# Kernel optimization log

Measured on AMD Instinct MI355X. Metric: run time of the kernel, lower is better.

The kernel has to match this reference:

```python
import jax, jax.numpy as jnp
import numpy as np

# --- fake-quant helpers with straight-through estimator (STE) ---

def _ste(x, xq):
    # identity grad through the rounding
    return x + jax.lax.stop_gradient(xq - x)

def act_quant(x, bit=2):
    # symmetric per-tensor uniform fake-quant of activations
    n = float(2 ** (bit - 1) - 1)  # 2-bit -> 1 level each side
    s = jnp.max(jnp.abs(x)) + 1e-8
    xq = jnp.round(jnp.clip(x / s, -1.0, 1.0) * n) / n * s
    return _ste(x, xq)

def weight_quant(w, bit=2):
    # DoReFa-style low-bit weight fake-quant
    levels = float(2 ** bit - 1)
    wt = jnp.tanh(w)
    wt = wt / (jnp.max(jnp.abs(wt)) + 1e-8)        # in [-1, 1]
    wq = 2.0 * (jnp.round((wt + 1.0) * 0.5 * levels) / levels) - 1.0
    return _ste(wt, wq)

def conv3x3(x, w, b):
    # NCHW, OIHW, stride 1, padding 1
    y = jax.lax.conv_general_dilated(
        x, w, window_strides=(1, 1), padding=((1, 1), (1, 1)),
        dimension_numbers=("NCHW", "OIHW", "NCHW"))
    return y + b[None, :, None, None]


def setup_inputs() -> dict:
    key = jax.random.key(0)
    k1, k2, k3, k4, k5 = jax.random.split(key, 5)
    B, C, H, W = 16, 64, 128, 128
    fan_in = C * 3 * 3
    std = 1.0 / np.sqrt(fan_in)
    return {
        "x": jax.random.normal(k1, (B, C, H, W), dtype=jnp.float32),
        "w1": jax.random.normal(k2, (C, C, 3, 3), dtype=jnp.float32) * std,
        "b1": jax.random.normal(k3, (C,), dtype=jnp.float32) * std,
        "w2": jax.random.normal(k4, (C, C, 3, 3), dtype=jnp.float32) * std,
        "b2": jax.random.normal(k5, (C,), dtype=jnp.float32) * std,
    }


def reference(x, w1, b1, w2, b2):
    A_BIT, W_BIT, RES_SCALE = 2, 2, 1.0
    out = act_quant(x, A_BIT)                 # quant1
    out = conv3x3(out, weight_quant(w1, W_BIT), b1)  # conv1 (low-bit)
    out1 = jax.nn.relu(out)                   # act
    out1 = act_quant(out1, A_BIT)             # quant2
    res = conv3x3(out1, weight_quant(w2, W_BIT), b2) # conv2 (low-bit)
    return res * RES_SCALE + x                # scaled residual add
```

## Files before the change

kernel.cpp:

```cpp
#include <hip/hip_runtime.h>
#include <math.h>

#define NB 16
#define CC 64
#define HH 128
#define WW 128
#define NPIX (NB*CC*HH*WW)
#define WELEM (CC*CC*9)

#define TR 16
#define TC 16
#define HR 18
#define HC 18
#define HPX (HR*HC)
#define PL  (HH*WW)

#define PYY 132
#define PXX 130
#define XQIMG (PYY*PXX*64)
#define XQTOT (NB*XQIMG)

#define S2OFF 512

typedef __attribute__((ext_vector_type(4))) int   int32x4;
typedef __attribute__((ext_vector_type(4))) short short4_t;
typedef __attribute__((ext_vector_type(8))) short short8_t;

__device__ __forceinline__ int lds_a(int pix, int q) {
    return pix * 64 + ((q ^ ((pix >> 1) & 3)) << 4);
}

__device__ __forceinline__ float read_s1(const unsigned* scal) {
    float m = 0.f;
    #pragma unroll
    for (int i = 0; i < 32; ++i) m = fmaxf(m, __uint_as_float(scal[i * 16]));
    return m + 1e-8f;
}

__device__ __forceinline__ float max4(float4 v) {
    return fmaxf(fmaxf(fabsf(v.x), fabsf(v.y)), fmaxf(fabsf(v.z), fabsf(v.w)));
}

__global__ __launch_bounds__(256) void k_reduce(const float* __restrict__ x,
                                                const float* __restrict__ w1,
                                                const float* __restrict__ w2,
                                                unsigned* __restrict__ scal,
                                                signed char* __restrict__ o1,
                                                signed char* __restrict__ o2) {
    __shared__ float red[4];
    const int tid = threadIdx.x;
    if (blockIdx.x < 2048) {
        const float4* x4 = (const float4*)x;
        const int base = blockIdx.x * 2048 + tid;
        float4 v0 = x4[base];
        float4 v1 = x4[base + 256];
        float4 v2 = x4[base + 512];
        float4 v3 = x4[base + 768];
        float4 v4 = x4[base + 1024];
        float4 v5 = x4[base + 1280];
        float4 v6 = x4[base + 1536];
        float4 v7 = x4[base + 1792];
        float a0 = fmaxf(max4(v0), max4(v1));
        float a1 = fmaxf(max4(v2), max4(v3));
        float a2 = fmaxf(max4(v4), max4(v5));
        float a3 = fmaxf(max4(v6), max4(v7));
        float m = fmaxf(fmaxf(a0, a1), fmaxf(a2, a3));
        #pragma unroll
        for (int o = 32; o; o >>= 1) m = fmaxf(m, __shfl_down(m, o, 64));
        if ((tid & 63) == 0) red[tid >> 6] = m;
        __syncthreads();
        if (tid == 0) {
            float v = fmaxf(fmaxf(red[0], red[1]), fmaxf(red[2], red[3]));
            atomicMax(&scal[(blockIdx.x & 31) * 16], __float_as_uint(v));
        }
    } else {
        const int wb = blockIdx.x - 2048;
        const int ten = wb >> 4;
        const int sl  = wb & 15;
        const float* __restrict__ w = ten ? w2 : w1;
        signed char* __restrict__ w8 = ten ? o2 : o1;

        const float4* w4 = (const float4*)w;
        float m = 0.f;
        #pragma unroll
        for (int k = 0; k < 9; ++k) {
            float4 a = w4[tid + (k * 4 + 0) * 256];
            float4 b = w4[tid + (k * 4 + 1) * 256];
            float4 c = w4[tid + (k * 4 + 2) * 256];
            float4 d = w4[tid + (k * 4 + 3) * 256];
            m = fmaxf(m, fmaxf(fmaxf(max4(a), max4(b)), fmaxf(max4(c), max4(d))));
        }
        #pragma unroll
        for (int o = 32; o; o >>= 1) m = fmaxf(m, __shfl_down(m, o, 64));
        if ((tid & 63) == 0) red[tid >> 6] = m;
        __syncthreads();
        float mx = fmaxf(fmaxf(red[0], red[1]), fmaxf(red[2], red[3]));
        float inv = 1.f / (tanhf(mx) + 1e-8f);

        #pragma unroll
        for (int j = 0; j < 9; ++j) {
            int i = sl * 2304 + j * 256 + tid;
            float wt = tanhf(w[i]) * inv;
            float r  = rintf((wt + 1.f) * 1.5f);
            int oc = i / 576, rem = i % 576, ic = rem / 9, tap = rem % 9;
            int lane2 = (oc & 15) | ((ic >> 4) << 4);
            w8[(((oc >> 4) * 9 + tap) * 64 + lane2) * 16 + (ic & 15)] =
                (signed char)(int)(2.f * r - 3.f);
        }
    }
}

__global__ __launch_bounds__(256) void k_quantx(const float* __restrict__ x,
                                                const unsigned* __restrict__ scal,
                                                signed char* __restrict__ xq) {
    __shared__ signed char ldsA[64 * 68];
    __shared__ int ldsB[64 * 16];
    const int tid = threadIdx.x;
    const int n = blockIdx.z, y = blockIdx.y, s = blockIdx.x;
    const float inv_s1 = 1.f / read_s1(scal);

    {
        const int ic = tid >> 2, g = tid & 3;
        const float* __restrict__ src =
            x + (((size_t)n * CC + ic) * HH + y) * WW + s * 64 + g * 16;
        unsigned dw[4];
        #pragma unroll
        for (int q = 0; q < 4; ++q) {
            float4 v = *(const float4*)(src + q * 4);
            float e[4] = {v.x, v.y, v.z, v.w};
            unsigned d = 0;
            #pragma unroll
            for (int j = 0; j < 4; ++j) {
                int qq = (int)rintf(fminf(fmaxf(e[j] * inv_s1, -1.f), 1.f));
                d |= (unsigned)(qq & 255) << (8 * j);
            }
            dw[q] = d;
        }
        *(int4*)(ldsA + ic * 68 + g * 16) = *(const int4*)dw;
    }
    __syncthreads();
    #pragma unroll
    for (int i = 0; i < 4; ++i) {
        int idx = tid + i * 256;
        int d = idx & 15, p = idx >> 4;
        const signed char* a = ldsA + (d * 4) * 68 + p;
        unsigned b0 = (unsigned char)a[0];
        unsigned b1 = (unsigned char)a[68];
        unsigned b2 = (unsigned char)a[136];
        unsigned b3 = (unsigned char)a[204];
        ldsB[p * 16 + d] = (int)(b0 | (b1 << 8) | (b2 << 16) | (b3 << 24));
    }
    __syncthreads();
    signed char* dst = xq + ((size_t)n * PYY + (y + 1)) * (PXX * 64)
                          + (size_t)(1 + s * 64) * 64;
    ((int4*)dst)[tid] = ((const int4*)ldsB)[tid];
}

__global__ __launch_bounds__(512, 5) void k_conv1(
    const signed char* __restrict__ xq,
    const signed char* __restrict__ w8,
    const float* __restrict__ bias,
    unsigned* __restrict__ scal,
    short* __restrict__ accout)
{
    __shared__ float redm[8];
    const int tid = threadIdx.x;
    const int n   = blockIdx.z;
    const int oy0 = blockIdx.y * TR;
    const int ox0 = blockIdx.x * TC;
    const float s1 = read_s1(scal);

    const int w     = tid >> 6;
    const int lane  = tid & 63;
    const int lq    = lane >> 4;
    const int lc    = lane & 15;
    const int mH    = w & 1;
    const int rbase = (w >> 1) * 4;

    const signed char* __restrict__ A0 = xq + (size_t)n * XQIMG
        + ((size_t)(oy0 + rbase) * PXX + ox0 + lc) * 64 + lq * 16;
    const signed char* __restrict__ W0 = w8 + ((size_t)mH * 18 * 64 + lane) * 16;

    int32x4 acc0[4] = {};
    int32x4 acc1[4] = {};
    #pragma unroll 3
    for (int tap = 0; tap < 9; ++tap) {
        const int ky = tap / 3, kx = tap % 3;
        int32x4 b0 = *(const int32x4*)(W0 + (size_t)tap * 1024);
        int32x4 b1 = *(const int32x4*)(W0 + (size_t)(9 + tap) * 1024);
        const signed char* ar = A0 + (ky * PXX + kx) * 64;
        #pragma unroll
        for (int j = 0; j < 4; ++j) {
            int32x4 a = *(const int32x4*)(ar + j * (PXX * 64));
            acc0[j] = __builtin_amdgcn_mfma_i32_16x16x64_i8(a, b0, acc0[j], 0, 0, 0);
            acc1[j] = __builtin_amdgcn_mfma_i32_16x16x64_i8(a, b1, acc1[j], 0, 0, 0);
        }
    }

    const float sc = s1 * (1.f / 3.f);
    const int oc0 = mH * 32 + lc;
    const int oc1 = oc0 + 16;
    const float bo0 = bias[oc0], bo1 = bias[oc1];
    const size_t abase = (((size_t)n * HH + (oy0 + rbase)) * WW + (ox0 + lq * 4)) * 64;

    float m2 = 0.f;
    #pragma unroll
    for (int j = 0; j < 4; ++j) {
        #pragma unroll
        for (int g = 0; g < 4; ++g) {
            int v0 = acc0[j][g], v1 = acc1[j][g];
            m2 = fmaxf(m2, sc * (float)v0 + bo0);
            m2 = fmaxf(m2, sc * (float)v1 + bo1);
            size_t a = abase + ((size_t)j * WW + g) * 64;
            accout[a + oc0] = (short)v0;
            accout[a + oc1] = (short)v1;
        }
    }
    #pragma unroll
    for (int o = 32; o; o >>= 1) m2 = fmaxf(m2, __shfl_down(m2, o, 64));
    if (lane == 0) redm[w] = m2;
    __syncthreads();
    if (tid == 0) {
        float v = redm[0];
        #pragma unroll
        for (int i = 1; i < 8; ++i) v = fmaxf(v, redm[i]);
        int slot = (blockIdx.x + blockIdx.y * 8 + blockIdx.z) & 7;
        atomicMax(&scal[S2OFF + slot * 32], __float_as_uint(v));
    }
}

__global__ __launch_bounds__(512, 5) void k_conv2(
    const float* __restrict__ x,
    const short* __restrict__ accin,
    const signed char* __restrict__ w8,
    const float* __restrict__ bias,
    const float* __restrict__ b1v,
    const unsigned* __restrict__ scal,
    float* __restrict__ out)
{
    __shared__ signed char sA[HPX * 64] __attribute__((aligned(16)));

    const int tid = threadIdx.x;
    const int n   = blockIdx.z;
    const int oy0 = blockIdx.y * TR;
    const int ox0 = blockIdx.x * TC;

    const float s1 = read_s1(scal);
    float mx = 0.f;
    #pragma unroll
    for (int i = 0; i < 8; ++i) mx = fmaxf(mx, __uint_as_float(scal[S2OFF + i * 32]));
    const float s2v = mx + 1e-8f;
    const float half_s2 = 0.5f * s2v;
    const float sc1 = s1 * (1.f / 3.f);

    for (int t = tid; t < HPX; t += 512) {
        const int r = t / HC, c = t - r * HC;
        const int y  = oy0 - 1 + r;
        const int xx = ox0 - 1 + c;
        unsigned pk[16];
        #pragma unroll
        for (int d = 0; d < 16; ++d) pk[d] = 0;
        if (y >= 0 && y < HH && xx >= 0 && xx < WW) {
            const short8_t* __restrict__ ap =
                (const short8_t*)(accin + (((size_t)n * HH + y) * WW + xx) * 64);
            #pragma unroll
            for (int k = 0; k < 8; ++k) {
                short8_t sv = ap[k];
                float4 bA = *(const float4*)(b1v + k * 8);
                float4 bB = *(const float4*)(b1v + k * 8 + 4);
                float ba[8] = {bA.x, bA.y, bA.z, bA.w, bB.x, bB.y, bB.z, bB.w};
                #pragma unroll
                for (int e = 0; e < 8; ++e) {
                    float fv = sc1 * (float)sv[e] + ba[e];
                    if (fv >= half_s2) pk[2 * k + (e >> 2)] |= 1u << ((e & 3) * 8);
                }
            }
        }
        #pragma unroll
        for (int q = 0; q < 4; ++q) {
            int4 wv;
            wv.x = (int)pk[4 * q];     wv.y = (int)pk[4 * q + 1];
            wv.z = (int)pk[4 * q + 2]; wv.w = (int)pk[4 * q + 3];
            *(int4*)(sA + lds_a(t, q)) = wv;
        }
    }
    __syncthreads();

    const int w     = tid >> 6;
    const int lane  = tid & 63;
    const int lq    = lane >> 4;
    const int lc    = lane & 15;
    const int mH    = w & 1;
    const int rbase = (w >> 1) * 4;
    const signed char* __restrict__ W0 = w8 + ((size_t)mH * 18 * 64 + lane) * 16;

    int32x4 acc0[4] = {};
    int32x4 acc1[4] = {};
    __builtin_amdgcn_s_setprio(1);
    #pragma unroll 3
    for (int tap = 0; tap < 9; ++tap) {
        const int ky = tap / 3, kx = tap % 3;
        int32x4 b0 = *(const int32x4*)(W0 + (size_t)tap * 1024);
        int32x4 b1 = *(const int32x4*)(W0 + (size_t)(9 + tap) * 1024);
        #pragma unroll
        for (int j = 0; j < 4; ++j) {
            int pix = (rbase + j + ky) * HC + kx + lc;
            int32x4 a = *(const int32x4*)(sA + lds_a(pix, lq));
            acc0[j] = __builtin_amdgcn_mfma_i32_16x16x64_i8(a, b0, acc0[j], 0, 0, 0);
            acc1[j] = __builtin_amdgcn_mfma_i32_16x16x64_i8(a, b1, acc1[j], 0, 0, 0);
        }
    }
    __builtin_amdgcn_s_setprio(0);

    const float sc = s2v * (1.f / 3.f);
    const int oc0 = mH * 32 + lc;
    const int oc1 = oc0 + 16;
    const float bo0 = bias[oc0], bo1 = bias[oc1];
    const size_t imgbase = (size_t)n * CC * PL;

    #pragma unroll
    for (int j = 0; j < 4; ++j) {
        int yy = oy0 + rbase + j;
        int xb = ox0 + lq * 4;
        size_t p0 = imgbase + (size_t)oc0 * PL + yy * WW + xb;
        size_t p1 = imgbase + (size_t)oc1 * PL + yy * WW + xb;
        float4 xa  = *(const float4*)(x + p0);
        float4 xb4 = *(const float4*)(x + p1);
        float4 r0, r1;
        r0.x = sc * (float)acc0[j][0] + bo0 + xa.x;
        r0.y = sc * (float)acc0[j][1] + bo0 + xa.y;
        r0.z = sc * (float)acc0[j][2] + bo0 + xa.z;
        r0.w = sc * (float)acc0[j][3] + bo0 + xa.w;
        r1.x = sc * (float)acc1[j][0] + bo1 + xb4.x;
        r1.y = sc * (float)acc1[j][1] + bo1 + xb4.y;
        r1.z = sc * (float)acc1[j][2] + bo1 + xb4.z;
        r1.w = sc * (float)acc1[j][3] + bo1 + xb4.w;
        *(float4*)(out + p0) = r0;
        *(float4*)(out + p1) = r1;
    }
}

extern "C" void kernel_launch(void* const* d_in, const int* in_sizes, int n_in,
                              void* d_out, int out_size, void* d_ws, size_t ws_size,
                              hipStream_t stream) {
    const float* x  = (const float*)d_in[0];
    const float* w1 = (const float*)d_in[1];
    const float* b1 = (const float*)d_in[2];
    const float* w2 = (const float*)d_in[3];
    const float* b2 = (const float*)d_in[4];
    float* out = (float*)d_out;

    unsigned*    scal  = (unsigned*)d_ws;
    signed char* w8_1  = (signed char*)d_ws + 4096;
    signed char* w8_2  = w8_1 + WELEM;
    short*       acc16 = (short*)((char*)d_ws + 131072);
    signed char* xq    = (signed char*)d_out;

    hipMemsetAsync(d_ws, 0, 4096, stream);
    hipMemsetAsync(d_out, 0, XQTOT, stream);

    k_reduce<<<2080, 256, 0, stream>>>(x, w1, w2, scal, w8_1, w8_2);
    k_quantx<<<dim3(2, HH, NB), 256, 0, stream>>>(x, scal, xq);

    dim3 grid(WW / TC, HH / TR, NB);
    k_conv1<<<grid, 512, 0, stream>>>(xq, w8_1, b1, scal, acc16);
    k_conv2<<<grid, 512, 0, stream>>>(x, acc16, w8_2, b2, b1, scal, out);
}
```

Baseline: 114.1 us.

## Shrink conv tiles to 8x16 with 256-thread blocks, each wave covering all 64 channels

```diff
diff --git a/kernel.cpp b/kernel.cpp
--- a/kernel.cpp
+++ b/kernel.cpp
@@ -8,11 +8,11 @@
 #define NPIX (NB*CC*HH*WW)
 #define WELEM (CC*CC*9)
 
-#define TR 16
-#define TC 16
-#define HR 18
-#define HC 18
-#define HPX (HR*HC)
+#define TRR 8
+#define TCC 16
+#define HRR 10
+#define HCC 18
+#define HPX (HRR*HCC)
 #define PL  (HH*WW)
 
 #define PYY 132
@@ -23,7 +23,6 @@
 #define S2OFF 512
 
 typedef __attribute__((ext_vector_type(4))) int   int32x4;
-typedef __attribute__((ext_vector_type(4))) short short4_t;
 typedef __attribute__((ext_vector_type(8))) short short8_t;
 
 __device__ __forceinline__ int lds_a(int pix, int q) {
@@ -156,64 +155,64 @@
     ((int4*)dst)[tid] = ((const int4*)ldsB)[tid];
 }
 
-__global__ __launch_bounds__(512, 5) void k_conv1(
+__global__ __launch_bounds__(256, 5) void k_conv1(
     const signed char* __restrict__ xq,
     const signed char* __restrict__ w8,
     const float* __restrict__ bias,
     unsigned* __restrict__ scal,
     short* __restrict__ accout)
 {
-    __shared__ float redm[8];
+    __shared__ float redm[4];
     const int tid = threadIdx.x;
     const int n   = blockIdx.z;
-    const int oy0 = blockIdx.y * TR;
-    const int ox0 = blockIdx.x * TC;
+    const int oy0 = blockIdx.y * TRR;
+    const int ox0 = blockIdx.x * TCC;
     const float s1 = read_s1(scal);
 
     const int w     = tid >> 6;
     const int lane  = tid & 63;
     const int lq    = lane >> 4;
     const int lc    = lane & 15;
-    const int mH    = w & 1;
-    const int rbase = (w >> 1) * 4;
+    const int rbase = w * 2;
 
     const signed char* __restrict__ A0 = xq + (size_t)n * XQIMG
         + ((size_t)(oy0 + rbase) * PXX + ox0 + lc) * 64 + lq * 16;
-    const signed char* __restrict__ W0 = w8 + ((size_t)mH * 18 * 64 + lane) * 16;
-
-    int32x4 acc0[4] = {};
-    int32x4 acc1[4] = {};
+    const signed char* __restrict__ W0 = w8 + (size_t)lane * 16;
+
+    int32x4 acc[2][4] = {};
     #pragma unroll 3
     for (int tap = 0; tap < 9; ++tap) {
         const int ky = tap / 3, kx = tap % 3;
-        int32x4 b0 = *(const int32x4*)(W0 + (size_t)tap * 1024);
-        int32x4 b1 = *(const int32x4*)(W0 + (size_t)(9 + tap) * 1024);
+        int32x4 b0 = *(const int32x4*)(W0 + (size_t)(0 * 9 + tap) * 1024);
+        int32x4 b1 = *(const int32x4*)(W0 + (size_t)(1 * 9 + tap) * 1024);
+        int32x4 b2 = *(const int32x4*)(W0 + (size_t)(2 * 9 + tap) * 1024);
+        int32x4 b3 = *(const int32x4*)(W0 + (size_t)(3 * 9 + tap) * 1024);
         const signed char* ar = A0 + (ky * PXX + kx) * 64;
         #pragma unroll
-        for (int j = 0; j < 4; ++j) {
+        for (int j = 0; j < 2; ++j) {
             int32x4 a = *(const int32x4*)(ar + j * (PXX * 64));
-            acc0[j] = __builtin_amdgcn_mfma_i32_16x16x64_i8(a, b0, acc0[j], 0, 0, 0);
-            acc1[j] = __builtin_amdgcn_mfma_i32_16x16x64_i8(a, b1, acc1[j], 0, 0, 0);
+            acc[j][0] = __builtin_amdgcn_mfma_i32_16x16x64_i8(a, b0, acc[j][0], 0, 0, 0);
+            acc[j][1] = __builtin_amdgcn_mfma_i32_16x16x64_i8(a, b1, acc[j][1], 0, 0, 0);
+            acc[j][2] = __builtin_amdgcn_mfma_i32_16x16x64_i8(a, b2, acc[j][2], 0, 0, 0);
+            acc[j][3] = __builtin_amdgcn_mfma_i32_16x16x64_i8(a, b3, acc[j][3], 0, 0, 0);
         }
     }
 
     const float sc = s1 * (1.f / 3.f);
-    const int oc0 = mH * 32 + lc;
-    const int oc1 = oc0 + 16;
-    const float bo0 = bias[oc0], bo1 = bias[oc1];
-    const size_t abase = (((size_t)n * HH + (oy0 + rbase)) * WW + (ox0 + lq * 4)) * 64;
-
     float m2 = 0.f;
     #pragma unroll
-    for (int j = 0; j < 4; ++j) {
+    for (int j = 0; j < 2; ++j) {
+        const int yy = oy0 + rbase + j;
+        const size_t pbase = (((size_t)n * HH + yy) * WW + (ox0 + lq * 4)) * 64;
         #pragma unroll
         for (int g = 0; g < 4; ++g) {
-            int v0 = acc0[j][g], v1 = acc1[j][g];
-            m2 = fmaxf(m2, sc * (float)v0 + bo0);
-            m2 = fmaxf(m2, sc * (float)v1 + bo1);
-            size_t a = abase + ((size_t)j * WW + g) * 64;
-            accout[a + oc0] = (short)v0;
-            accout[a + oc1] = (short)v1;
+            const float bo = bias[g * 16 + lc];
+            #pragma unroll
+            for (int e = 0; e < 4; ++e) {
+                int v = acc[j][g][e];
+                m2 = fmaxf(m2, sc * (float)v + bo);
+                accout[pbase + (size_t)e * 64 + g * 16 + lc] = (short)v;
+            }
         }
     }
     #pragma unroll
@@ -221,15 +220,13 @@
     if (lane == 0) redm[w] = m2;
     __syncthreads();
     if (tid == 0) {
-        float v = redm[0];
-        #pragma unroll
-        for (int i = 1; i < 8; ++i) v = fmaxf(v, redm[i]);
+        float v = fmaxf(fmaxf(redm[0], redm[1]), fmaxf(redm[2], redm[3]));
         int slot = (blockIdx.x + blockIdx.y * 8 + blockIdx.z) & 7;
         atomicMax(&scal[S2OFF + slot * 32], __float_as_uint(v));
     }
 }
 
-__global__ __launch_bounds__(512, 5) void k_conv2(
+__global__ __launch_bounds__(256, 5) void k_conv2(
     const float* __restrict__ x,
     const short* __restrict__ accin,
     const signed char* __restrict__ w8,
@@ -242,8 +239,8 @@
 
     const int tid = threadIdx.x;
     const int n   = blockIdx.z;
-    const int oy0 = blockIdx.y * TR;
-    const int ox0 = blockIdx.x * TC;
+    const int oy0 = blockIdx.y * TRR;
+    const int ox0 = blockIdx.x * TCC;
 
     const float s1 = read_s1(scal);
     float mx = 0.f;
@@ -253,8 +250,8 @@
     const float half_s2 = 0.5f * s2v;
     const float sc1 = s1 * (1.f / 3.f);
 
-    for (int t = tid; t < HPX; t += 512) {
-        const int r = t / HC, c = t - r * HC;
+    if (tid < HPX) {
+        const int r = tid / HCC, c = tid - r * HCC;
         const int y  = oy0 - 1 + r;
         const int xx = ox0 - 1 + c;
         unsigned pk[16];
@@ -281,7 +278,7 @@
             int4 wv;
             wv.x = (int)pk[4 * q];     wv.y = (int)pk[4 * q + 1];
             wv.z = (int)pk[4 * q + 2]; wv.w = (int)pk[4 * q + 3];
-            *(int4*)(sA + lds_a(t, q)) = wv;
+            *(int4*)(sA + lds_a(tid, q)) = wv;
         }
     }
     __syncthreads();
@@ -290,53 +287,50 @@
     const int lane  = tid & 63;
     const int lq    = lane >> 4;
     const int lc    = lane & 15;
-    const int mH    = w & 1;
-    const int rbase = (w >> 1) * 4;
-    const signed char* __restrict__ W0 = w8 + ((size_t)mH * 18 * 64 + lane) * 16;
-
-    int32x4 acc0[4] = {};
-    int32x4 acc1[4] = {};
+    const int rbase = w * 2;
+    const signed char* __restrict__ W0 = w8 + (size_t)lane * 16;
+
+    int32x4 acc[2][4] = {};
     __builtin_amdgcn_s_setprio(1);
     #pragma unroll 3
     for (int tap = 0; tap < 9; ++tap) {
         const int ky = tap / 3, kx = tap % 3;
-        int32x4 b0 = *(const int32x4*)(W0 + (size_t)tap * 1024);
-        int32x4 b1 = *(const int32x4*)(W0 + (size_t)(9 + tap) * 1024);
-        #pragma unroll
-        for (int j = 0; j < 4; ++j) {
-            int pix = (rbase + j + ky) * HC + kx + lc;
+        int32x4 b0 = *(const int32x4*)(W0 + (size_t)(0 * 9 + tap) * 1024);
+        int32x4 b1 = *(const int32x4*)(W0 + (size_t)(1 * 9 + tap) * 1024);
+        int32x4 b2 = *(const int32x4*)(W0 + (size_t)(2 * 9 + tap) * 1024);
+        int32x4 b3 = *(const int32x4*)(W0 + (size_t)(3 * 9 + tap) * 1024);
+        #pragma unroll
+        for (int j = 0; j < 2; ++j) {
+            int pix = (rbase + j + ky) * HCC + kx + lc;
             int32x4 a = *(const int32x4*)(sA + lds_a(pix, lq));
-            acc0[j] = __builtin_amdgcn_mfma_i32_16x16x64_i8(a, b0, acc0[j], 0, 0, 0);
-            acc1[j] = __builtin_amdgcn_mfma_i32_16x16x64_i8(a, b1, acc1[j], 0, 0, 0);
+            acc[j][0] = __builtin_amdgcn_mfma_i32_16x16x64_i8(a, b0, acc[j][0], 0, 0, 0);
+            acc[j][1] = __builtin_amdgcn_mfma_i32_16x16x64_i8(a, b1, acc[j][1], 0, 0, 0);
+            acc[j][2] = __builtin_amdgcn_mfma_i32_16x16x64_i8(a, b2, acc[j][2], 0, 0, 0);
+            acc[j][3] = __builtin_amdgcn_mfma_i32_16x16x64_i8(a, b3, acc[j][3], 0, 0, 0);
         }
     }
     __builtin_amdgcn_s_setprio(0);
 
     const float sc = s2v * (1.f / 3.f);
-    const int oc0 = mH * 32 + lc;
-    const int oc1 = oc0 + 16;
-    const float bo0 = bias[oc0], bo1 = bias[oc1];
     const size_t imgbase = (size_t)n * CC * PL;
 
     #pragma unroll
-    for (int j = 0; j < 4; ++j) {
-        int yy = oy0 + rbase + j;
-        int xb = ox0 + lq * 4;
-        size_t p0 = imgbase + (size_t)oc0 * PL + yy * WW + xb;
-        size_t p1 = imgbase + (size_t)oc1 * PL + yy * WW + xb;
-        float4 xa  = *(const float4*)(x + p0);
-        float4 xb4 = *(const float4*)(x + p1);
-        float4 r0, r1;
-        r0.x = sc * (float)acc0[j][0] + bo0 + xa.x;
-        r0.y = sc * (float)acc0[j][1] + bo0 + xa.y;
-        r0.z = sc * (float)acc0[j][2] + bo0 + xa.z;
-        r0.w = sc * (float)acc0[j][3] + bo0 + xa.w;
-        r1.x = sc * (float)acc1[j][0] + bo1 + xb4.x;
-        r1.y = sc * (float)acc1[j][1] + bo1 + xb4.y;
-        r1.z = sc * (float)acc1[j][2] + bo1 + xb4.z;
-        r1.w = sc * (float)acc1[j][3] + bo1 + xb4.w;
-        *(float4*)(out + p0) = r0;
-        *(float4*)(out + p1) = r1;
+    for (int j = 0; j < 2; ++j) {
+        const int yy = oy0 + rbase + j;
+        const int xb = ox0 + lq * 4;
+        #pragma unroll
+        for (int g = 0; g < 4; ++g) {
+            const int oc = g * 16 + lc;
+            const float bo = bias[oc];
+            size_t p = imgbase + (size_t)oc * PL + yy * WW + xb;
+            float4 xa = *(const float4*)(x + p);
+            float4 r;
+            r.x = sc * (float)acc[j][g][0] + bo + xa.x;
+            r.y = sc * (float)acc[j][g][1] + bo + xa.y;
+            r.z = sc * (float)acc[j][g][2] + bo + xa.z;
+            r.w = sc * (float)acc[j][g][3] + bo + xa.w;
+            *(float4*)(out + p) = r;
+        }
     }
 }
 
@@ -362,7 +356,7 @@
     k_reduce<<<2080, 256, 0, stream>>>(x, w1, w2, scal, w8_1, w8_2);
     k_quantx<<<dim3(2, HH, NB), 256, 0, stream>>>(x, scal, xq);
 
-    dim3 grid(WW / TC, HH / TR, NB);
-    k_conv1<<<grid, 512, 0, stream>>>(xq, w8_1, b1, scal, acc16);
-    k_conv2<<<grid, 512, 0, stream>>>(x, acc16, w8_2, b2, b1, scal, out);
-}
+    dim3 grid(WW / TCC, HH / TRR, NB);
+    k_conv1<<<grid, 256, 0, stream>>>(xq, w8_1, b1, scal, acc16);
+    k_conv2<<<grid, 256, 0, stream>>>(x, acc16, w8_2, b2, b1, scal, out);
+}
```

New measurement: 114.8 us. No clear change (+0.6%).
